# Kernel optimization log

Measured on AMD Instinct MI355X. Metric: run time of the kernel, lower is better.

The kernel has to match this reference:

```python
import jax, jax.numpy as jnp
from jax import lax
import numpy as np

B, T, I, H, L, O = 256, 512, 1, 256, 4, 1


def setup_inputs() -> dict:
    key = jax.random.key(0)
    ks = jax.random.split(key, 4 * L + 3)
    s = 1.0 / np.sqrt(H)
    inp = {"x": jax.random.normal(ks[0], (B, T, I), dtype=jnp.float32)}
    for l in range(L):
        in_dim = I if l == 0 else H
        inp[f"W_ih{l}"] = jax.random.uniform(ks[1 + 4 * l], (4 * H, in_dim), minval=-s, maxval=s, dtype=jnp.float32)
        inp[f"W_hh{l}"] = jax.random.uniform(ks[2 + 4 * l], (4 * H, H), minval=-s, maxval=s, dtype=jnp.float32)
        inp[f"b_ih{l}"] = jax.random.uniform(ks[3 + 4 * l], (4 * H,), minval=-s, maxval=s, dtype=jnp.float32)
        inp[f"b_hh{l}"] = jax.random.uniform(ks[4 + 4 * l], (4 * H,), minval=-s, maxval=s, dtype=jnp.float32)
    inp["fc_W"] = jax.random.uniform(ks[-2], (O, H), minval=-s, maxval=s, dtype=jnp.float32)
    inp["fc_b"] = jax.random.uniform(ks[-1], (O,), minval=-s, maxval=s, dtype=jnp.float32)
    return inp


def _lstm_layer(x_seq, W_ih, W_hh, b_ih, b_hh):
    # x_seq: [B, T, in_dim] -> hidden sequence [B, T, H]
    b, t = x_seq.shape[0], x_seq.shape[1]
    h = W_hh.shape[1]
    # precompute input projections for all timesteps: [T, B, 4H]
    xg = jnp.einsum('bti,gi->tbg', x_seq, W_ih) + b_ih + b_hh

    def step(carry, xg_t):
        hp, cp = carry
        gates = xg_t + hp @ W_hh.T  # [B, 4H]
        i, f, g, o = jnp.split(gates, 4, axis=-1)  # PyTorch gate order: i,f,g,o
        i = jax.nn.sigmoid(i)
        f = jax.nn.sigmoid(f)
        g = jnp.tanh(g)
        o = jax.nn.sigmoid(o)
        c = f * cp + i * g
        hn = o * jnp.tanh(c)
        return (hn, c), hn

    h0 = jnp.zeros((b, h), x_seq.dtype)
    _, hs = lax.scan(step, (h0, h0), xg)
    return jnp.transpose(hs, (1, 0, 2))  # [B, T, H]


def reference(x, W_ih0, W_hh0, b_ih0, b_hh0, W_ih1, W_hh1, b_ih1, b_hh1,
              W_ih2, W_hh2, b_ih2, b_hh2, W_ih3, W_hh3, b_ih3, b_hh3, fc_W, fc_b):
    layers = [(W_ih0, W_hh0, b_ih0, b_hh0), (W_ih1, W_hh1, b_ih1, b_hh1),
              (W_ih2, W_hh2, b_ih2, b_hh2), (W_ih3, W_hh3, b_ih3, b_hh3)]
    out = x
    for Wi, Wh, bi, bh in layers:
        out = _lstm_layer(out, Wi, Wh, bi, bh)
    # final linear on last timestep hidden: [B, H] -> [B, O]
    return out[:, -1, :] @ fc_W.T + fc_b
```

## Files before the change

### kernel.cpp

```cpp
#include <hip/hip_runtime.h>
#include <stdint.h>

#define T_ 512
#define H_ 256
#define MB 32
#define NBUF 8
#define ISLOT 8192
#define NWG 256

typedef __attribute__((ext_vector_type(8))) short  short8;
typedef __attribute__((ext_vector_type(4))) float  floatx4;
typedef __attribute__((ext_vector_type(4))) unsigned int uint4v;
typedef unsigned long long ull;

struct Params {
  const float* x;
  const float* Wih[4]; const float* Whh[4]; const float* bih[4]; const float* bhh[4];
  const float* fcW; const float* fcb;
  int*   flags;
  int*   xcd;
  short* hring;
};

__device__ __forceinline__ short f2bf(float f){
  uint32_t u = __builtin_bit_cast(uint32_t, f);
  u += 0x7fffu + ((u >> 16) & 1u);
  return (short)(u >> 16);
}
__device__ __forceinline__ float bf2f(short s){
  uint32_t u = ((uint32_t)(uint16_t)s) << 16;
  return __builtin_bit_cast(float, u);
}
__device__ __forceinline__ float sigm(float v){ return 1.0f / (1.0f + __expf(-v)); }
__device__ __forceinline__ float tanh_(float v){
  float a = fabsf(v);
  float e = __expf(-2.0f * a);
  float r = (1.0f - e) / (1.0f + e);
  return v < 0.0f ? -r : r;
}

__device__ __forceinline__ void a_st32(unsigned* p, unsigned v){
  __hip_atomic_store(p, v, __ATOMIC_RELAXED, __HIP_MEMORY_SCOPE_AGENT);
}
__device__ __forceinline__ int a_ldi(const int* p){
  return __hip_atomic_load(p, __ATOMIC_RELAXED, __HIP_MEMORY_SCOPE_AGENT);
}
__device__ __forceinline__ void a_sti(int* p, int v){
  __hip_atomic_store(p, v, __ATOMIC_RELAXED, __HIP_MEMORY_SCOPE_AGENT);
}

template<bool SL> __device__ __forceinline__ void ld16t(uint4v& d, const void* p){
  if constexpr (SL) asm volatile("global_load_dwordx4 %0, %1, off sc0 sc1" : "=v"(d) : "v"(p));
  else              asm volatile("global_load_dwordx4 %0, %1, off sc0"     : "=v"(d) : "v"(p));
}
template<bool SL> __device__ __forceinline__ void st32t(unsigned* p, unsigned v){
  if constexpr (SL) a_st32(p, v);
  else asm volatile("global_store_dword %0, %1, off sc0" :: "v"(p), "v"(v) : "memory");
}
__device__ __forceinline__ void inv_l1(){
  asm volatile("buffer_inv sc0" ::: "memory");
}

__device__ __forceinline__ void ldf32(float& d, const void* p){
  asm volatile("global_load_dword %0, %1, off" : "=v"(d) : "v"(p));
}
template<int N> __device__ __forceinline__ void waitvm(){
  if constexpr (N == 0) asm volatile("s_waitcnt vmcnt(0)" ::: "memory");
  else if constexpr (N == 1) asm volatile("s_waitcnt vmcnt(1)" ::: "memory");
  else                       asm volatile("s_waitcnt vmcnt(4)" ::: "memory");
}
__device__ __forceinline__ void bar_lds(){
  asm volatile("s_waitcnt lgkmcnt(0)" ::: "memory");
  __builtin_amdgcn_s_barrier();
}
__device__ __forceinline__ void bar_only(){
  __builtin_amdgcn_s_barrier();
}

#define MFMA(a,b,c) __builtin_amdgcn_mfma_f32_16x16x32_bf16((a),(b),(c),0,0,0)

__device__ __forceinline__ void wpoll(const int* p, int thr, bool& dead){
  if (dead) return;
  int guard = 0;
  for (;;){
    int v = a_ldi(p);
    if (__all((int)(v >= thr))) break;
    if (++guard > (1 << 16)) { dead = true; break; }
  }
}

template<bool L0, bool SL>
__device__ __forceinline__ void run_cell(const Params& p, int g, int l, int slice,
    short* a_frag, float (*g_lds)[MB][33], float (*bias_lds)[32],
    float (*wih0_lds)[32], float* x0_lds)
{
  constexpr int KBT = L0 ? 8 : 16;
  const int tid = threadIdx.x, lane = tid & 63, wave = tid >> 6;
  const int n15 = lane & 15, q4 = lane >> 4;

  int* fl_self = p.flags + (g * 4 + l) * 32;
  int* fl_up   = L0 ? fl_self : fl_self - 32;
  int* fl_down = (l < 3) ? fl_self + 32 : fl_self;
  short* hr_self = p.hring + (size_t)((g * 4 + l) * NBUF) * ISLOT;
  const short* hr_up = L0 ? (const short*)nullptr
                          : hr_self - (size_t)NBUF * ISLOT;

  if (tid < 128){
    int gt = tid >> 5, j = tid & 31;
    int gr = gt * 256 + slice * 32 + j;
    bias_lds[gt][j] = p.bih[l][gr] + p.bhh[l][gr];
    if (L0) wih0_lds[gt][j] = p.Wih[0][gr];
  }

  short8 wf0[KBT], wf1[KBT];
  const int g0 = wave * 256 + slice * 32 + n15;
  const int g1 = g0 + 16;
  #pragma unroll
  for (int kb = 0; kb < KBT; ++kb){
    const float* base; int kk;
    if (L0)          { base = p.Whh[0]; kk = kb * 32 + q4 * 8; }
    else if (kb < 8) { base = p.Wih[l]; kk = kb * 32 + q4 * 8; }
    else             { base = p.Whh[l]; kk = (kb - 8) * 32 + q4 * 8; }
    const float* p0 = base + (size_t)g0 * H_ + kk;
    const float* p1 = base + (size_t)g1 * H_ + kk;
    short8 a, b;
    #pragma unroll
    for (int i = 0; i < 8; ++i){ a[i] = f2bf(p0[i]); b[i] = f2bf(p1[i]); }
    wf0[kb] = a; wf1[kb] = b;
  }

  float c00 = 0.f, c01 = 0.f, c10 = 0.f, c11 = 0.f;
  const int r0 = (tid >> 4) * 2, r1 = r0 + 1;
  const int pc = (tid & 15) * 2;

  const int* pp; int dlt;
  if (lane < 8)      { pp = fl_self + lane; dlt = 0; }
  else if (lane < 16){ if (L0){ pp = fl_self; dlt = -1000000; }
                       else   { pp = fl_up + (lane - 8); dlt = 2; } }
  else if (lane < 24){ if (l < 3){ pp = fl_down + (lane - 16); dlt = -7; }
                       else      { pp = fl_self; dlt = -1000000; } }
  else               { pp = fl_self + (lane & 7); dlt = -1000000; }
  bool dead = false;

  uint4v* fragv = (uint4v*)a_frag;
  uint4v px[4];
  float xcur = 0.f;

  if (!L0){
    wpoll(fl_up + (lane & 7), 1, dead);
    if constexpr (!SL) inv_l1();
    const char* s = (const char*)hr_up;
    #pragma unroll
    for (int k = 0; k < 4; ++k) ld16t<SL>(px[k], s + (size_t)(k * 256 + tid) * 16);
  } else if (wave == 0 && lane < MB){
    ldf32(xcur, &p.x[(size_t)(g * MB + lane) * T_]);
  }
  waitvm<0>();
  __syncthreads();

  for (int t = 0; t < T_; ++t){
    { int thr = t + dlt; if (thr > T_) thr = T_;
      wpoll(pp, thr, dead); }
    if constexpr (!SL) inv_l1();

    if (!L0){
      #pragma unroll
      for (int k = 0; k < 4; ++k) fragv[k * 256 + tid] = px[k];
    } else if (wave == 0 && lane < MB){
      x0_lds[lane] = xcur;
    }

    uint4v hv[4];
    const bool havh = (t > 0);
    const bool pf = (t + 1 < T_);
    if (havh){
      const char* s = (const char*)(hr_self + (size_t)((t - 1) & 7) * ISLOT);
      #pragma unroll
      for (int k = 0; k < 4; ++k) ld16t<SL>(hv[k], s + (size_t)(k * 256 + tid) * 16);
    }
    if (!L0){
      if (pf){
        const char* s = (const char*)(hr_up + (size_t)((t + 1) & 7) * ISLOT);
        #pragma unroll
        for (int k = 0; k < 4; ++k) ld16t<SL>(px[k], s + (size_t)(k * 256 + tid) * 16);
      }
    } else if (wave == 0 && lane < MB && pf){
      ldf32(xcur, &p.x[(size_t)(g * MB + lane) * T_ + (t + 1)]);
    }

    bar_lds();

    floatx4 acc[2][2][2] = {};
    if (!L0){
      #pragma unroll
      for (int kb = 0; kb < 8; ++kb){
        #pragma unroll
        for (int mt = 0; mt < 2; ++mt){
          short8 af = *(short8*)&a_frag[(kb * 2 + mt) * 512 + lane * 8];
          int pr = kb & 1;
          acc[mt][0][pr] = MFMA(af, wf0[kb], acc[mt][0][pr]);
          acc[mt][1][pr] = MFMA(af, wf1[kb], acc[mt][1][pr]);
        }
      }
    }

    if (!L0){ if (pf) waitvm<4>(); else waitvm<0>(); }
    else    { if (wave == 0 && pf) waitvm<1>(); else waitvm<0>(); }
    {
      const int hbase = L0 ? 0 : 1024;
      if (havh){
        #pragma unroll
        for (int k = 0; k < 4; ++k) fragv[hbase + k * 256 + tid] = hv[k];
      } else {
        uint4v z = {0, 0, 0, 0};
        #pragma unroll
        for (int k = 0; k < 4; ++k) fragv[hbase + k * 256 + tid] = z;
      }
    }
    bar_lds();

    #pragma unroll
    for (int kb = (L0 ? 0 : 8); kb < KBT; ++kb){
      #pragma unroll
      for (int mt = 0; mt < 2; ++mt){
        short8 af = *(short8*)&a_frag[(kb * 2 + mt) * 512 + lane * 8];
        int pr = kb & 1;
        acc[mt][0][pr] = MFMA(af, wf0[kb], acc[mt][0][pr]);
        acc[mt][1][pr] = MFMA(af, wf1[kb], acc[mt][1][pr]);
      }
    }
    #pragma unroll
    for (int mt = 0; mt < 2; ++mt){
      floatx4 s0 = acc[mt][0][0] + acc[mt][0][1];
      floatx4 s1 = acc[mt][1][0] + acc[mt][1][1];
      int mrow = mt * 16 + q4 * 4;
      #pragma unroll
      for (int r = 0; r < 4; ++r){
        g_lds[wave][mrow + r][n15]      = s0[r];
        g_lds[wave][mrow + r][16 + n15] = s1[r];
      }
    }
    bar_lds();

    {
      float xs0 = 0.f, xs1 = 0.f;
      if (L0){ xs0 = x0_lds[r0]; xs1 = x0_lds[r1]; }
      short* slot = hr_self + (size_t)(t & 7) * ISLOT;
      #pragma unroll
      for (int rr = 0; rr < 2; ++rr){
        const int row = rr ? r1 : r0;
        const float xs = rr ? xs1 : xs0;
        float gi0 = g_lds[0][row][pc]   + bias_lds[0][pc];
        float gi1 = g_lds[0][row][pc+1] + bias_lds[0][pc+1];
        float gf0 = g_lds[1][row][pc]   + bias_lds[1][pc];
        float gf1 = g_lds[1][row][pc+1] + bias_lds[1][pc+1];
        float gg0 = g_lds[2][row][pc]   + bias_lds[2][pc];
        float gg1 = g_lds[2][row][pc+1] + bias_lds[2][pc+1];
        float go0 = g_lds[3][row][pc]   + bias_lds[3][pc];
        float go1 = g_lds[3][row][pc+1] + bias_lds[3][pc+1];
        if (L0){
          gi0 += xs * wih0_lds[0][pc]; gi1 += xs * wih0_lds[0][pc+1];
          gf0 += xs * wih0_lds[1][pc]; gf1 += xs * wih0_lds[1][pc+1];
          gg0 += xs * wih0_lds[2][pc]; gg1 += xs * wih0_lds[2][pc+1];
          go0 += xs * wih0_lds[3][pc]; go1 += xs * wih0_lds[3][pc+1];
        }
        float i0 = sigm(gi0), i1 = sigm(gi1);
        float f0 = sigm(gf0), f1 = sigm(gf1);
        float gv0 = tanh_(gg0), gv1 = tanh_(gg1);
        float o0 = sigm(go0), o1 = sigm(go1);
        float& ca = rr ? c10 : c00;
        float& cb = rr ? c11 : c01;
        ca = f0 * ca + i0 * gv0;
        cb = f1 * cb + i1 * gv1;
        float h0 = o0 * tanh_(ca);
        float h1 = o1 * tanh_(cb);
        unsigned pk = (unsigned)(uint16_t)f2bf(h0) | ((unsigned)(uint16_t)f2bf(h1) << 16);
        unsigned off = (unsigned)((slice * 2 + (row >> 4)) * 512
                     + ((pc >> 3) * 16 + (row & 15)) * 8 + (pc & 7));
        st32t<SL>((unsigned*)(slot + off), pk);
      }
    }

    waitvm<0>();
    bar_only();
    if (tid == 0) a_sti(fl_self + slice, t + 1);
  }
}

__global__ __launch_bounds__(256, 1) void lstm_kernel(Params p){
  __shared__ short a_frag[32 * 512];
  __shared__ float g_lds[4][MB][33];
  __shared__ float bias_lds[4][32];
  __shared__ float wih0_lds[4][32];
  __shared__ float x0_lds[MB];
  __shared__ int   fsh;

  const int bid   = blockIdx.x;
  const int g     = bid & 7;
  const int l     = (bid >> 3) & 3;
  const int slice = bid >> 5;

  int xcc;
  asm volatile("s_getreg_b32 %0, hwreg(HW_REG_XCC_ID)" : "=s"(xcc));
  const int me = xcc + 1;
  if (threadIdx.x == 0) a_sti(&p.xcd[bid], me);
  int fast;
  {
    const int lane = threadIdx.x & 63;
    const int idx = lane & 31;
    const int* xp = p.xcd + (idx >> 2) * 32 + (idx & 3) * 8 + g;
    int v = 0, guard = 0; bool giveup = false;
    for (;;){
      v = a_ldi(xp);
      if (__all((int)(v != 0))) break;
      if (++guard > (1 << 22)) { giveup = true; break; }
    }
    fast = (!giveup && __all((int)(v == me))) ? 1 : 0;
  }
  if (threadIdx.x == 0) fsh = 1;
  __syncthreads();
  if (!fast) fsh = 0;
  __syncthreads();
  fast = fsh;

  if (l == 0){
    if (fast) run_cell<true , false>(p, g, 0, slice, a_frag, g_lds, bias_lds, wih0_lds, x0_lds);
    else      run_cell<true , true >(p, g, 0, slice, a_frag, g_lds, bias_lds, wih0_lds, x0_lds);
  } else {
    if (fast) run_cell<false, false>(p, g, l, slice, a_frag, g_lds, bias_lds, wih0_lds, x0_lds);
    else      run_cell<false, true >(p, g, l, slice, a_frag, g_lds, bias_lds, wih0_lds, x0_lds);
  }
}

__global__ void fc_kernel(const short* __restrict__ hring, const float* __restrict__ fcW,
                          const float* __restrict__ fcb, float* __restrict__ out){
  int b = blockIdx.x, lane = threadIdx.x;
  int g = b >> 5, m = b & 31;
  int mt = m >> 4, mm = m & 15;
  const short* base = hring + (size_t)((g * 4 + 3) * NBUF + ((T_ - 1) & 7)) * ISLOT;
  float s = 0.f;
  #pragma unroll
  for (int k = 0; k < 4; ++k){
    int d = lane + 64 * k;
    int kb = d >> 5, koff = d & 31;
    short hv = base[(kb * 2 + mt) * 512 + ((koff >> 3) * 16 + mm) * 8 + (koff & 7)];
    s += bf2f(hv) * fcW[d];
  }
  #pragma unroll
  for (int off = 32; off; off >>= 1) s += __shfl_down(s, off);
  if (lane == 0) out[b] = s + fcb[0];
}

extern "C" void kernel_launch(void* const* d_in, const int* in_sizes, int n_in,
                              void* d_out, int out_size, void* d_ws, size_t ws_size,
                              hipStream_t stream) {
  Params P;
  P.x = (const float*)d_in[0];
  for (int l = 0; l < 4; ++l){
    P.Wih[l] = (const float*)d_in[1 + 4*l];
    P.Whh[l] = (const float*)d_in[2 + 4*l];
    P.bih[l] = (const float*)d_in[3 + 4*l];
    P.bhh[l] = (const float*)d_in[4 + 4*l];
  }
  P.fcW = (const float*)d_in[17];
  P.fcb = (const float*)d_in[18];

  char* ws = (char*)d_ws;
  P.flags = (int*)ws;
  P.xcd   = (int*)(ws + 4096);
  P.hring = (short*)(ws + 16384);

  hipMemsetAsync(ws, 0, 8192, stream);
  hipLaunchKernelGGL(lstm_kernel, dim3(NWG), dim3(256), 0, stream, P);
  hipLaunchKernelGGL(fc_kernel, dim3(256), dim3(64), 0, stream,
                     P.hring, P.fcW, P.fcb, (float*)d_out);
}
```

Before: 1.850 ms.

## Replace per-slice flag polling with atomic counters in same-XCD path

In the non-SL (same-XCD) path, the eight per-slice step flags become a single atomic counter per (group, layer). Each workgroup increments it after every step, and wave 0 polls the self, upstream and downstream counters with three lanes using atomic-add-zero reads. The L1 invalidate now happens after the barrier and just before the ring loads are issued. This is meant to cut the number of polled locations and make the cross-workgroup handshake cheaper. The cost is L2 atomic contention on one counter and an extra barrier before the loads start.

```diff
diff --git a/kernel.cpp b/kernel.cpp
--- a/kernel.cpp
+++ b/kernel.cpp
@@ -49,6 +49,18 @@
   __hip_atomic_store(p, v, __ATOMIC_RELAXED, __HIP_MEMORY_SCOPE_AGENT);
 }
 
+__device__ __forceinline__ int ctr_poll(const int* p){
+  int v; int z = 0;
+  asm volatile("global_atomic_add %0, %1, %2, off sc0\n\t"
+               "s_waitcnt vmcnt(0)"
+               : "=v"(v) : "v"(p), "v"(z) : "memory");
+  return v;
+}
+__device__ __forceinline__ void ctr_post(int* p){
+  int one = 1;
+  asm volatile("global_atomic_add %0, %1, off" :: "v"(p), "v"(one) : "memory");
+}
+
 template<bool SL> __device__ __forceinline__ void ld16t(uint4v& d, const void* p){
   if constexpr (SL) asm volatile("global_load_dwordx4 %0, %1, off sc0 sc1" : "=v"(d) : "v"(p));
   else              asm volatile("global_load_dwordx4 %0, %1, off sc0"     : "=v"(d) : "v"(p));
@@ -84,6 +96,24 @@
   int guard = 0;
   for (;;){
     int v = a_ldi(p);
+    if (__all((int)(v >= thr))) break;
+    if (++guard > (1 << 16)) { dead = true; break; }
+  }
+}
+
+__device__ __forceinline__ void cpoll(const int* self, const int* up, const int* down,
+                                      int t, bool& dead){
+  if (dead) return;
+  const int lane = threadIdx.x & 63;
+  const int* p = nullptr; int thr = 0;
+  if (lane == 0)            { p = self; thr = t; }
+  else if (lane == 1 && up) { p = up;   thr = t + 2; }
+  else if (lane == 2 && down){ p = down; thr = t - 7; }
+  if (thr > T_) thr = T_;
+  thr <<= 3;
+  int guard = 0;
+  for (;;){
+    int v = p ? ctr_poll(p) : 0x7fffffff;
     if (__all((int)(v >= thr))) break;
     if (++guard > (1 << 16)) { dead = true; break; }
   }
@@ -104,6 +134,10 @@
   short* hr_self = p.hring + (size_t)((g * 4 + l) * NBUF) * ISLOT;
   const short* hr_up = L0 ? (const short*)nullptr
                           : hr_self - (size_t)NBUF * ISLOT;
+
+  int* ctr_self = fl_self;
+  const int* ctr_up   = L0 ? (const int*)nullptr : fl_self - 32;
+  const int* ctr_down = (l < 3) ? fl_self + 32 : (const int*)nullptr;
 
   if (tid < 128){
     int gt = tid >> 5, j = tid & 31;
@@ -147,8 +181,13 @@
   float xcur = 0.f;
 
   if (!L0){
-    wpoll(fl_up + (lane & 7), 1, dead);
-    if constexpr (!SL) inv_l1();
+    if constexpr (SL){
+      wpoll(fl_up + (lane & 7), 1, dead);
+    } else {
+      if (wave == 0) cpoll(ctr_self, ctr_up, ctr_down, -1, dead);
+      __syncthreads();
+      inv_l1();
+    }
     const char* s = (const char*)hr_up;
     #pragma unroll
     for (int k = 0; k < 4; ++k) ld16t<SL>(px[k], s + (size_t)(k * 256 + tid) * 16);
@@ -159,9 +198,12 @@
   __syncthreads();
 
   for (int t = 0; t < T_; ++t){
-    { int thr = t + dlt; if (thr > T_) thr = T_;
-      wpoll(pp, thr, dead); }
-    if constexpr (!SL) inv_l1();
+    if constexpr (SL){
+      int thr = t + dlt; if (thr > T_) thr = T_;
+      wpoll(pp, thr, dead);
+    } else {
+      if (wave == 0) cpoll(ctr_self, ctr_up, ctr_down, t, dead);
+    }
 
     if (!L0){
       #pragma unroll
@@ -173,22 +215,31 @@
     uint4v hv[4];
     const bool havh = (t > 0);
     const bool pf = (t + 1 < T_);
-    if (havh){
-      const char* s = (const char*)(hr_self + (size_t)((t - 1) & 7) * ISLOT);
-      #pragma unroll
-      for (int k = 0; k < 4; ++k) ld16t<SL>(hv[k], s + (size_t)(k * 256 + tid) * 16);
-    }
-    if (!L0){
-      if (pf){
-        const char* s = (const char*)(hr_up + (size_t)((t + 1) & 7) * ISLOT);
+    auto issue_loads = [&](){
+      if (havh){
+        const char* s = (const char*)(hr_self + (size_t)((t - 1) & 7) * ISLOT);
         #pragma unroll
-        for (int k = 0; k < 4; ++k) ld16t<SL>(px[k], s + (size_t)(k * 256 + tid) * 16);
-      }
-    } else if (wave == 0 && lane < MB && pf){
-      ldf32(xcur, &p.x[(size_t)(g * MB + lane) * T_ + (t + 1)]);
-    }
-
-    bar_lds();
+        for (int k = 0; k < 4; ++k) ld16t<SL>(hv[k], s + (size_t)(k * 256 + tid) * 16);
+      }
+      if (!L0){
+        if (pf){
+          const char* s = (const char*)(hr_up + (size_t)((t + 1) & 7) * ISLOT);
+          #pragma unroll
+          for (int k = 0; k < 4; ++k) ld16t<SL>(px[k], s + (size_t)(k * 256 + tid) * 16);
+        }
+      } else if (wave == 0 && lane < MB && pf){
+        ldf32(xcur, &p.x[(size_t)(g * MB + lane) * T_ + (t + 1)]);
+      }
+    };
+
+    if constexpr (SL){
+      issue_loads();
+      bar_lds();
+    } else {
+      bar_lds();
+      inv_l1();
+      issue_loads();
+    }
 
     floatx4 acc[2][2][2] = {};
     if (!L0){
@@ -283,7 +334,10 @@
 
     waitvm<0>();
     bar_only();
-    if (tid == 0) a_sti(fl_self + slice, t + 1);
+    if (tid == 0){
+      if constexpr (SL) a_sti(fl_self + slice, t + 1);
+      else              ctr_post(ctr_self);
+    }
   }
 }
 
```

Result: faster. 1.658 ms (-10.4%).
